# Kernel tuning notes

Hardware: AMD Instinct MI355X
Metric: run time of the kernel (lower is better)

## Reference

```python
import jax, jax.numpy as jnp
import numpy as np

N_NODES = 50000
N_EDGES = 800000
IN_FEAT = 512
HIDDEN = 64
N_CLASS = 16


def setup_inputs() -> dict:
    key = jax.random.key(0)
    ks = jax.random.split(key, 8)
    x = jax.random.normal(ks[0], (N_NODES, IN_FEAT), dtype=jnp.float32)
    src = jax.random.randint(ks[1], (N_EDGES,), 0, N_NODES, dtype=jnp.int32)
    dst = jax.random.randint(ks[2], (N_EDGES,), 0, N_NODES, dtype=jnp.int32)
    edge_weight = jax.random.uniform(ks[3], (N_EDGES,), dtype=jnp.float32)
    # Glorot-ish init for layer weights (GraphConvolution weight + bias)
    W1 = jax.random.normal(ks[4], (IN_FEAT, HIDDEN), dtype=jnp.float32) * (1.0 / np.sqrt(IN_FEAT))
    b1 = jnp.zeros((HIDDEN,), dtype=jnp.float32)
    W2 = jax.random.normal(ks[5], (HIDDEN, N_CLASS), dtype=jnp.float32) * (1.0 / np.sqrt(HIDDEN))
    b2 = jnp.zeros((N_CLASS,), dtype=jnp.float32)
    return {"x": x, "src": src, "dst": dst, "edge_weight": edge_weight,
            "W1": W1, "b1": b1, "W2": W2, "b2": b2}


def _spmm(src, dst, edge_weight, h):
    # sparse adj @ h via gather + weighted segment_sum over destination nodes
    msgs = h[src] * edge_weight[:, None]          # [E, d]
    return jax.ops.segment_sum(msgs, dst, num_segments=N_NODES)  # [N, d]


def reference(x, src, dst, edge_weight, W1, b1, W2, b2):
    # Layer 1: relu(adj @ (x @ W1) + b1)
    h = _spmm(src, dst, edge_weight, x @ W1) + b1   # [N, HIDDEN]
    h = jax.nn.relu(h)
    # Dropout is identity at inference (predict uses training=False).
    # Layer 2: softmax(adj @ (h @ W2) + b2)
    logits = _spmm(src, dst, edge_weight, h @ W2) + b2  # [N, N_CLASS]
    return jax.nn.softmax(logits, axis=-1)
```

## Files before the change

kernel.cpp:

```cpp
#include <hip/hip_runtime.h>

#define IN_FEAT 512
#define HIDDEN 64
#define N_CLASS 16
#define CAP 64

typedef __attribute__((ext_vector_type(8))) short bf16x8;
typedef __attribute__((ext_vector_type(8))) unsigned short ushort8;
typedef __attribute__((ext_vector_type(4))) float f32x4;

struct EdgeRec { int s; float w; };

__device__ inline unsigned short f2bf(float f) {
    union { float f; unsigned int u; } x; x.f = f;
    unsigned int u = x.u + 0x7FFFu + ((x.u >> 16) & 1u);
    return (unsigned short)(u >> 16);
}

__global__ __launch_bounds__(256) void k_init(const float* __restrict__ W1,
                                              unsigned short* __restrict__ bfrag,
                                              int* __restrict__ deg, int n) {
    int bid = blockIdx.x;
    if (bid < 16) {
        int t = bid * 256 + threadIdx.x;
        int l = t & 63;
        int grp = t >> 6;
        int ct = grp & 3, kc = grp >> 2;
        int k0 = kc * 32 + (l >> 4) * 8;
        int col = ct * 16 + (l & 15);
        ushort8 v;
#pragma unroll
        for (int j = 0; j < 8; ++j) v[j] = f2bf(W1[(k0 + j) * HIDDEN + col]);
        ((ushort8*)bfrag)[t] = v;
    } else {
        int i = (bid - 16) * 256 + threadIdx.x;
        if (i < n) deg[i] = 0;
    }
}

__global__ __launch_bounds__(256) void k_fused(const float* __restrict__ x,
                                               const unsigned short* __restrict__ bfrag,
                                               float* __restrict__ h0,
                                               const int* __restrict__ src,
                                               const int* __restrict__ dst,
                                               const float* __restrict__ ew,
                                               int* __restrict__ deg,
                                               EdgeRec* __restrict__ recs,
                                               int n, int E, int gb) {
    int bid = blockIdx.x;
    if (bid < gb) {
        int wid  = bid * 4 + (threadIdx.x >> 6);
        int lane = threadIdx.x & 63;
        int r0 = wid * 16;
        if (r0 >= n) return;
        const float* xp = x + (size_t)(r0 + (lane & 15)) * IN_FEAT + (lane >> 4) * 8;

        bf16x8 afr[16];
#pragma unroll
        for (int kc = 0; kc < 16; ++kc) {
            f32x4 a0 = *(const f32x4*)(xp + kc * 32);
            f32x4 a1 = *(const f32x4*)(xp + kc * 32 + 4);
            bf16x8 a;
#pragma unroll
            for (int j = 0; j < 4; ++j) a[j] = (short)f2bf(a0[j]);
#pragma unroll
            for (int j = 0; j < 4; ++j) a[4 + j] = (short)f2bf(a1[j]);
            afr[kc] = a;
        }

        const bf16x8* B = (const bf16x8*)bfrag;
        f32x4 acc0 = {0,0,0,0}, acc1 = {0,0,0,0}, acc2 = {0,0,0,0}, acc3 = {0,0,0,0};
#pragma unroll
        for (int kc = 0; kc < 16; ++kc) {
            bf16x8 b0 = B[(kc * 4 + 0) * 64 + lane];
            bf16x8 b1 = B[(kc * 4 + 1) * 64 + lane];
            bf16x8 b2 = B[(kc * 4 + 2) * 64 + lane];
            bf16x8 b3 = B[(kc * 4 + 3) * 64 + lane];
            acc0 = __builtin_amdgcn_mfma_f32_16x16x32_bf16(afr[kc], b0, acc0, 0, 0, 0);
            acc1 = __builtin_amdgcn_mfma_f32_16x16x32_bf16(afr[kc], b1, acc1, 0, 0, 0);
            acc2 = __builtin_amdgcn_mfma_f32_16x16x32_bf16(afr[kc], b2, acc2, 0, 0, 0);
            acc3 = __builtin_amdgcn_mfma_f32_16x16x32_bf16(afr[kc], b3, acc3, 0, 0, 0);
        }

        int c = lane & 15;
        int rb = r0 + ((lane >> 4) << 2);
#pragma unroll
        for (int j = 0; j < 4; ++j) {
            float* o = h0 + (size_t)(rb + j) * HIDDEN;
            o[ 0 + c] = acc0[j];
            o[16 + c] = acc1[j];
            o[32 + c] = acc2[j];
            o[48 + c] = acc3[j];
        }
    } else {
        int i = (bid - gb) * 256 + threadIdx.x;
        if (i < E) {
            int d = dst[i];
            int r = atomicAdd(&deg[d], 1);
            if (r < CAP) {
                EdgeRec rec; rec.s = src[i]; rec.w = ew[i];
                recs[(size_t)d * CAP + r] = rec;
            }
        }
    }
}

__global__ __launch_bounds__(256) void k_spmm1g2(const int* __restrict__ deg,
                                                 const EdgeRec* __restrict__ recs,
                                                 const float* __restrict__ h0,
                                                 const float* __restrict__ b1,
                                                 const float* __restrict__ W2,
                                                 float* __restrict__ h2, int n) {
    int wid  = blockIdx.x * 4 + (threadIdx.x >> 6);
    int lane = threadIdx.x & 63;
    if (wid >= n) return;
    int node = __builtin_amdgcn_readfirstlane(wid);
    int cnt = deg[node]; if (cnt > CAP) cnt = CAP;
    const EdgeRec* er = recs + (size_t)node * CAP;
    float acc = 0.f;
    for (int e = 0; e < cnt; ++e) {
        EdgeRec r = er[e];
        acc = fmaf(r.w, h0[(size_t)r.s * HIDDEN + lane], acc);
    }
    float h1v = acc + b1[lane];
    h1v = h1v > 0.f ? h1v : 0.f;

    int f  = lane & 15;
    int kb = lane & 48;
    float sum = 0.f;
#pragma unroll
    for (int j = 0; j < 16; ++j) {
        float hk = __shfl(h1v, kb + j, 64);
        sum = fmaf(hk, W2[(kb + j) * N_CLASS + f], sum);
    }
    sum += __shfl_xor(sum, 16, 64);
    sum += __shfl_xor(sum, 32, 64);
    if (lane < 16) h2[(size_t)node * N_CLASS + lane] = sum;
}

__global__ __launch_bounds__(256) void k_spmm2(const int* __restrict__ deg,
                                               const EdgeRec* __restrict__ recs,
                                               const float* __restrict__ h2,
                                               const float* __restrict__ b2,
                                               float* __restrict__ out, int n) {
    int wid  = blockIdx.x * 4 + (threadIdx.x >> 6);
    int lane = threadIdx.x & 63;
    int node = wid * 4 + (lane >> 4);
    int f    = lane & 15;
    if (node >= n) return;
    int cnt = deg[node]; if (cnt > CAP) cnt = CAP;
    const EdgeRec* er = recs + (size_t)node * CAP;
    float acc = 0.f;
    for (int e = 0; e < cnt; ++e) {
        EdgeRec r = er[e];
        acc = fmaf(r.w, h2[(size_t)r.s * N_CLASS + f], acc);
    }
    float logit = acc + b2[f];
    float m = logit;
#pragma unroll
    for (int d = 1; d < 16; d <<= 1) m = fmaxf(m, __shfl_xor(m, d, 16));
    float ex = __expf(logit - m);
    float s = ex;
#pragma unroll
    for (int d = 1; d < 16; d <<= 1) s += __shfl_xor(s, d, 16);
    out[(size_t)node * N_CLASS + f] = ex / s;
}

extern "C" void kernel_launch(void* const* d_in, const int* in_sizes, int n_in,
                              void* d_out, int out_size, void* d_ws, size_t ws_size,
                              hipStream_t stream) {
    const float* x   = (const float*)d_in[0];
    const int*   src = (const int*)d_in[1];
    const int*   dst = (const int*)d_in[2];
    const float* ew  = (const float*)d_in[3];
    const float* W1  = (const float*)d_in[4];
    const float* b1  = (const float*)d_in[5];
    const float* W2  = (const float*)d_in[6];
    const float* b2  = (const float*)d_in[7];
    float* out = (float*)d_out;

    int n = in_sizes[0] / IN_FEAT;
    int E = in_sizes[1];

    float*   h0   = (float*)d_ws;
    float*   h2   = h0 + (size_t)n * HIDDEN;
    EdgeRec* recs = (EdgeRec*)(h2 + (size_t)n * N_CLASS);
    int*     deg  = (int*)(recs + (size_t)n * CAP);
    unsigned short* bfrag = (unsigned short*)(deg + n);

    int nb = (n + 255) / 256;
    int eb = (E + 255) / 256;
    int gb = ((n + 15) / 16 + 3) / 4;

    k_init<<<16 + nb, 256, 0, stream>>>(W1, bfrag, deg, n);
    k_fused<<<gb + eb, 256, 0, stream>>>(x, bfrag, h0, src, dst, ew, deg, recs, n, E, gb);
    k_spmm1g2<<<(n + 3) / 4, 256, 0, stream>>>(deg, recs, h0, b1, W2, h2, n);
    k_spmm2<<<(n + 15) / 16, 256, 0, stream>>>(deg, recs, h2, b2, out, n);
}
```

Measured before the change: 293.0 us.

## Batch edge-record loads per wave and unroll gathers in both SpMM kernels

```diff
diff --git a/kernel.cpp b/kernel.cpp
--- a/kernel.cpp
+++ b/kernel.cpp
@@ -117,21 +117,45 @@
     int node = __builtin_amdgcn_readfirstlane(wid);
     int cnt = deg[node]; if (cnt > CAP) cnt = CAP;
     const EdgeRec* er = recs + (size_t)node * CAP;
-    float acc = 0.f;
-    for (int e = 0; e < cnt; ++e) {
-        EdgeRec r = er[e];
-        acc = fmaf(r.w, h0[(size_t)r.s * HIDDEN + lane], acc);
-    }
-    float h1v = acc + b1[lane];
-    h1v = h1v > 0.f ? h1v : 0.f;
+
+    EdgeRec myr = {0, 0.f};
+    if (lane < cnt) myr = er[lane];
 
     int f  = lane & 15;
     int kb = lane & 48;
+    float bias = b1[lane];
+    float w2r[16];
+#pragma unroll
+    for (int j = 0; j < 16; ++j) w2r[j] = W2[(kb + j) * N_CLASS + f];
+
+    float acc = 0.f;
+    for (int e = 0; e < cnt; e += 8) {
+#define STEP(k)                                              \
+        int   s##k = __shfl(myr.s, e + k, 64);               \
+        float w##k = __shfl(myr.w, e + k, 64);               \
+        bool  p##k = (e + k < cnt);                          \
+        s##k = p##k ? s##k : 0;                              \
+        w##k = p##k ? w##k : 0.f;                            \
+        float g##k = h0[(size_t)s##k * HIDDEN + lane];
+        STEP(0) STEP(1) STEP(2) STEP(3) STEP(4) STEP(5) STEP(6) STEP(7)
+#undef STEP
+        acc = fmaf(w0, g0, acc);
+        acc = fmaf(w1, g1, acc);
+        acc = fmaf(w2, g2, acc);
+        acc = fmaf(w3, g3, acc);
+        acc = fmaf(w4, g4, acc);
+        acc = fmaf(w5, g5, acc);
+        acc = fmaf(w6, g6, acc);
+        acc = fmaf(w7, g7, acc);
+    }
+    float h1v = acc + bias;
+    h1v = h1v > 0.f ? h1v : 0.f;
+
     float sum = 0.f;
 #pragma unroll
     for (int j = 0; j < 16; ++j) {
         float hk = __shfl(h1v, kb + j, 64);
-        sum = fmaf(hk, W2[(kb + j) * N_CLASS + f], sum);
+        sum = fmaf(hk, w2r[j], sum);
     }
     sum += __shfl_xor(sum, 16, 64);
     sum += __shfl_xor(sum, 32, 64);
@@ -145,17 +169,33 @@
                                                float* __restrict__ out, int n) {
     int wid  = blockIdx.x * 4 + (threadIdx.x >> 6);
     int lane = threadIdx.x & 63;
-    int node = wid * 4 + (lane >> 4);
-    int f    = lane & 15;
-    if (node >= n) return;
+    if (wid >= n) return;
+    int node = __builtin_amdgcn_readfirstlane(wid);
     int cnt = deg[node]; if (cnt > CAP) cnt = CAP;
     const EdgeRec* er = recs + (size_t)node * CAP;
+
+    EdgeRec myr = {0, 0.f};
+    if (lane < cnt) myr = er[lane];
+
+    int f = lane & 15;
+    int q = lane >> 4;
+    float bias = b2[f];
+
     float acc = 0.f;
-    for (int e = 0; e < cnt; ++e) {
-        EdgeRec r = er[e];
-        acc = fmaf(r.w, h2[(size_t)r.s * N_CLASS + f], acc);
-    }
-    float logit = acc + b2[f];
+#pragma unroll
+    for (int i = 0; i < 16; ++i) {
+        int e = 4 * i + q;
+        int   s = __shfl(myr.s, e, 64);
+        float w = __shfl(myr.w, e, 64);
+        bool  p = (e < cnt);
+        s = p ? s : 0;
+        w = p ? w : 0.f;
+        acc = fmaf(w, h2[(size_t)s * N_CLASS + f], acc);
+    }
+    acc += __shfl_xor(acc, 16, 64);
+    acc += __shfl_xor(acc, 32, 64);
+
+    float logit = acc + bias;
     float m = logit;
 #pragma unroll
     for (int d = 1; d < 16; d <<= 1) m = fmaxf(m, __shfl_xor(m, d, 16));
@@ -163,7 +203,7 @@
     float s = ex;
 #pragma unroll
     for (int d = 1; d < 16; d <<= 1) s += __shfl_xor(s, d, 16);
-    out[(size_t)node * N_CLASS + f] = ex / s;
+    if (lane < 16) out[(size_t)node * N_CLASS + lane] = ex / s;
 }
 
 extern "C" void kernel_launch(void* const* d_in, const int* in_sizes, int n_in,
@@ -195,5 +235,5 @@
     k_init<<<16 + nb, 256, 0, stream>>>(W1, bfrag, deg, n);
     k_fused<<<gb + eb, 256, 0, stream>>>(x, bfrag, h0, src, dst, ew, deg, recs, n, E, gb);
     k_spmm1g2<<<(n + 3) / 4, 256, 0, stream>>>(deg, recs, h0, b1, W2, h2, n);
-    k_spmm2<<<(n + 15) / 16, 256, 0, stream>>>(deg, recs, h2, b2, out, n);
-}
+    k_spmm2<<<(n + 3) / 4, 256, 0, stream>>>(deg, recs, h2, b2, out, n);
+}
```

After: 271.3 us. -7.4%, faster.
